# Performance work log

Hardware: AMD Instinct MI355X
Metric: run time of the kernel (lower is better)

## Reference

```python
import jax, jax.numpy as jnp
import numpy as np

B, T, E, H = 16, 4096, 384, 64

def setup_inputs() -> dict:
    key = jax.random.key(0)
    k1, k2, k3, k4 = jax.random.split(key, 4)
    x = jax.random.normal(k1, (B, T, E), dtype=jnp.float32)
    # nn.Linear default init ~ U(-1/sqrt(fan_in), 1/sqrt(fan_in)); scale normals similarly
    s = 1.0 / np.sqrt(E)
    Wk = jax.random.uniform(k2, (E, H), dtype=jnp.float32, minval=-s, maxval=s)
    Wq = jax.random.uniform(k3, (E, H), dtype=jnp.float32, minval=-s, maxval=s)
    Wv = jax.random.uniform(k4, (E, H), dtype=jnp.float32, minval=-s, maxval=s)
    return {"x": x, "Wk": Wk, "Wq": Wq, "Wv": Wv}

def reference(x, Wk, Wq, Wv):
    b, t, c = x.shape
    k = x @ Wk          # [b,t,h]
    q = x @ Wq          # [b,t,h]
    v = x @ Wv          # [b,t,h]
    # scale by C**-0.5 where C is the embedding dim (as in source)
    scale = c ** (-0.5)
    weights = jnp.einsum('bqh,bkh->bqk', q, k) * scale  # [b,t,t]
    causal = jnp.tril(jnp.ones((t, t), dtype=bool))
    weights = jnp.where(causal, weights, -jnp.inf)
    weights = jax.nn.softmax(weights, axis=-1)
    # dropout is identity in eval mode
    out = jnp.einsum('bqk,bkh->bqh', weights, v)          # [b,t,h]
    return out
```

## Files before the change

kernel.cpp:

```cpp
#include <hip/hip_runtime.h>
#include <hip/hip_bf16.h>
#include <math.h>


typedef __attribute__((ext_vector_type(4))) float f32x4;
typedef __attribute__((ext_vector_type(8))) __bf16 bf16x8;

#define DEVI static __device__ __forceinline__

DEVI unsigned short f2bf(float f) {
  union { float f; unsigned int u; } x; x.f = f;
  unsigned int r = x.u + 0x7fffu + ((x.u >> 16) & 1u);
  return (unsigned short)(r >> 16);
}

DEVI unsigned int cvtpk_bf16(float lo, float hi) {
  unsigned int r;
  asm("v_cvt_pk_bf16_f32 %0, %1, %2" : "=v"(r) : "v"(lo), "v"(hi));
  return r;
}

DEVI f32x4 mfma16(bf16x8 a, bf16x8 b, f32x4 c) {
  return __builtin_amdgcn_mfma_f32_16x16x32_bf16(a, b, c, 0, 0, 0);
}

DEVI bf16x8 lds_frag(const unsigned short* buf, int row, int gran) {
  return *(const bf16x8*)(buf + row * 64 + ((gran ^ (row & 7)) << 3));
}

DEVI void gl_lds16(const unsigned short* g, unsigned short* l) {
  __builtin_amdgcn_global_load_lds(
      (const __attribute__((address_space(1))) unsigned int*)g,
      (__attribute__((address_space(3))) unsigned int*)l, 16, 0, 0);
}

__global__ __launch_bounds__(256) void k_pack(const float* __restrict__ Wk,
                                              const float* __restrict__ Wq,
                                              const float* __restrict__ Wv,
                                              unsigned short* __restrict__ WT) {
  int idx = blockIdx.x * 256 + threadIdx.x;
  if (idx >= 192 * 384) return;
  int n = idx / 384, k = idx - n * 384;
  const float* W = (n < 64) ? Wk : ((n < 128) ? Wq : Wv);
  WT[idx] = f2bf(W[k * 64 + (n & 63)]);
}

__global__ __launch_bounds__(256, 4) void k_proj(const float* __restrict__ x,
                                                 const unsigned short* __restrict__ WT,
                                                 unsigned short* __restrict__ Y,
                                                 unsigned short* __restrict__ VT) {
  __shared__ __align__(16) unsigned short As[64 * 64];
  __shared__ __align__(16) unsigned short Bs[192 * 64];
  const int tid = threadIdx.x;
  const int lane = tid & 63, wid = tid >> 6;
  const int q = lane & 15, g = lane >> 4;
  const int wm = wid >> 1, wn = wid & 1;
  const int m0 = blockIdx.x * 64;

  f32x4 acc[2][6];
#pragma unroll
  for (int mt = 0; mt < 2; ++mt)
#pragma unroll
    for (int nt = 0; nt < 6; ++nt) acc[mt][nt] = f32x4{0.f, 0.f, 0.f, 0.f};

  const int ar = tid >> 2, ap = tid & 3;

  for (int ks = 0; ks < 6; ++ks) {
    const float4* xp = (const float4*)(x + (size_t)(m0 + ar) * 384 + ks * 64 + ap * 16);
#pragma unroll
    for (int cc = 0; cc < 2; ++cc) {
      float4 f0 = xp[cc * 2], f1 = xp[cc * 2 + 1];
      union { unsigned short h[8]; uint4 v; } u;
      u.h[0] = f2bf(f0.x); u.h[1] = f2bf(f0.y); u.h[2] = f2bf(f0.z); u.h[3] = f2bf(f0.w);
      u.h[4] = f2bf(f1.x); u.h[5] = f2bf(f1.y); u.h[6] = f2bf(f1.z); u.h[7] = f2bf(f1.w);
      int gran = ap * 2 + cc;
      *(uint4*)(As + ar * 64 + ((gran ^ (ar & 7)) << 3)) = u.v;
    }
#pragma unroll
    for (int i = 0; i < 6; ++i) {
      int c = tid + 256 * i;
      int row = c >> 3, gr = c & 7;
      uint4 w = *(const uint4*)(WT + (size_t)row * 384 + ks * 64 + gr * 8);
      *(uint4*)(Bs + row * 64 + ((gr ^ (row & 7)) << 3)) = w;
    }
    __syncthreads();
#pragma unroll
    for (int kk = 0; kk < 2; ++kk) {
      bf16x8 af[2], bfv[6];
#pragma unroll
      for (int mt = 0; mt < 2; ++mt) af[mt] = lds_frag(As, wm * 32 + mt * 16 + q, kk * 4 + g);
#pragma unroll
      for (int nt = 0; nt < 6; ++nt) bfv[nt] = lds_frag(Bs, wn * 96 + nt * 16 + q, kk * 4 + g);
#pragma unroll
      for (int mt = 0; mt < 2; ++mt)
#pragma unroll
        for (int nt = 0; nt < 6; ++nt) acc[mt][nt] = mfma16(af[mt], bfv[nt], acc[mt][nt]);
    }
    __syncthreads();
  }
#pragma unroll
  for (int mt = 0; mt < 2; ++mt) {
    const int mrow = m0 + wm * 32 + mt * 16 + g * 4;
#pragma unroll
    for (int nt = 0; nt < 6; ++nt) {
      const int ncol = wn * 96 + nt * 16 + q;
      if (wn == 1 && nt >= 2) {
        const int d = (nt - 2) * 16 + q;
        const int bb = mrow >> 12, t = mrow & 4095;
        uint2 pv;
        pv.x = cvtpk_bf16(acc[mt][nt][0], acc[mt][nt][1]);
        pv.y = cvtpk_bf16(acc[mt][nt][2], acc[mt][nt][3]);
        *(uint2*)(VT + (size_t)(bb * 64 + d) * 4096 + t) = pv;
      } else {
        size_t base = (size_t)mrow * 128 + ncol;
#pragma unroll
        for (int j = 0; j < 4; ++j) Y[base + (size_t)j * 128] = f2bf(acc[mt][nt][j]);
      }
    }
  }
}

__global__ __launch_bounds__(512, 4) void k_attn(const unsigned short* __restrict__ Y,
                                                 const unsigned short* __restrict__ VT,
                                                 float* __restrict__ out) {
  __shared__ __align__(16) unsigned short Ks[4][64 * 64];
  __shared__ __align__(16) unsigned short Vs[4][64 * 64];
  __shared__ __align__(16) unsigned short Ps[8][16 * 64];

  const int id = blockIdx.x;
  const int xcd = id & 7;
  const int b = xcd * 2 + ((id >> 3) & 1);
  const int rank = id >> 4;
  const int i = (rank < 16) ? (31 - rank) : (rank - 16);
  const int q0 = i * 128;
  const int nkv = 2 * i + 2;

  const int tid = threadIdx.x;
  const int lane = tid & 63, wid = tid >> 6;
  const int p = wid >> 2;
  const int w4 = wid & 3;
  const int q = lane & 15, g = lane >> 4;
  const float zsc = 0.073622223f;

  const unsigned short* Yb = Y + (size_t)b * 4096 * 128;
  const unsigned short* Vb = VT + (size_t)b * 64 * 4096;

#define STAGE(S, KV0)                                                           \
  {                                                                             \
    int r = tid >> 3, grs = (tid & 7) ^ (r & 7);                                \
    gl_lds16(Yb + (size_t)((KV0) + r) * 128 + grs * 8, Ks[S] + tid * 8);        \
    gl_lds16(Vb + (size_t)r * 4096 + (KV0) + grs * 8, Vs[S] + tid * 8);         \
  }

  STAGE(0, 0)
  STAGE(1, 64)
  __syncthreads();

  bf16x8 qf[2][2];
#pragma unroll
  for (int qh = 0; qh < 2; ++qh) {
    const unsigned short* qp = Yb + (size_t)(q0 + w4 * 32 + qh * 16 + q) * 128 + 64;
    bf16x8 r0 = *(const bf16x8*)(qp + g * 8);
    bf16x8 r1 = *(const bf16x8*)(qp + 32 + g * 8);
#pragma unroll
    for (int e = 0; e < 8; ++e) {
      r0[e] = (__bf16)((float)r0[e] * zsc);
      r1[e] = (__bf16)((float)r1[e] * zsc);
    }
    qf[qh][0] = r0; qf[qh][1] = r1;
  }

  f32x4 accO[2][4];
#pragma unroll
  for (int qh = 0; qh < 2; ++qh)
#pragma unroll
    for (int dt = 0; dt < 4; ++dt) accO[qh][dt] = f32x4{0.f, 0.f, 0.f, 0.f};
  float lsum[2] = {0.f, 0.f};

  const int mytiles = 2 * i + 1 + (w4 >> 1);
  const int nIt = nkv >> 1;

  for (int it = 0; it < nIt; ++it) {
    const int kt = 2 * it + p;
    const int t2 = 2 * it + 2, t3 = 2 * it + 3;
    if (t2 < nkv) STAGE(t2 & 3, t2 * 64)
    if (t3 < nkv) STAGE(t3 & 3, t3 * 64)

    if (kt < mytiles) {
      const int kv0 = kt * 64;
      const unsigned short* Kc = Ks[kt & 3];
      const unsigned short* Vc = Vs[kt & 3];

      bf16x8 ka0[4], ka1[4];
#pragma unroll
      for (int t = 0; t < 4; ++t) {
        ka0[t] = lds_frag(Kc, t * 16 + q, g);
        ka1[t] = lds_frag(Kc, t * 16 + q, 4 + g);
      }
      f32x4 accS[2][4];
      __builtin_amdgcn_s_setprio(1);
#pragma unroll
      for (int qh = 0; qh < 2; ++qh)
#pragma unroll
        for (int t = 0; t < 4; ++t) {
          f32x4 z = f32x4{0.f, 0.f, 0.f, 0.f};
          z = mfma16(ka0[t], qf[qh][0], z);
          z = mfma16(ka1[t], qf[qh][1], z);
          accS[qh][t] = z;
        }
      __builtin_amdgcn_s_setprio(0);

      const bool dmw = (kv0 + 63 >= q0 + w4 * 32);
      bf16x8 bp[2][2];
#pragma unroll
      for (int qh = 0; qh < 2; ++qh) {
        const int qrow = q0 + w4 * 32 + qh * 16 + q;
        if (dmw) {
#pragma unroll
          for (int t = 0; t < 4; ++t)
#pragma unroll
            for (int j = 0; j < 4; ++j)
              if (kv0 + t * 16 + g * 4 + j > qrow) accS[qh][t][j] = -INFINITY;
        }
        float ps0 = 0.f, ps1 = 0.f;
#pragma unroll
        for (int t = 0; t < 4; ++t) {
          float p0 = __builtin_amdgcn_exp2f(accS[qh][t][0]);
          float p1 = __builtin_amdgcn_exp2f(accS[qh][t][1]);
          float p2 = __builtin_amdgcn_exp2f(accS[qh][t][2]);
          float p3 = __builtin_amdgcn_exp2f(accS[qh][t][3]);
          ps0 += p0 + p1;
          ps1 += p2 + p3;
          uint2 pv;
          pv.x = cvtpk_bf16(p0, p1);
          pv.y = cvtpk_bf16(p2, p3);
          *(uint2*)(Ps[wid] + q * 64 + ((t * 16 + g * 4) ^ ((q & 7) << 3))) = pv;
        }
        lsum[qh] += ps0 + ps1;
        bp[qh][0] = lds_frag(Ps[wid], q, g);
        bp[qh][1] = lds_frag(Ps[wid], q, 4 + g);
      }

      __builtin_amdgcn_s_setprio(1);
#pragma unroll
      for (int dt = 0; dt < 4; ++dt) {
        bf16x8 av0 = lds_frag(Vc, dt * 16 + q, g);
        bf16x8 av1 = lds_frag(Vc, dt * 16 + q, 4 + g);
#pragma unroll
        for (int qh = 0; qh < 2; ++qh) {
          accO[qh][dt] = mfma16(av0, bp[qh][0], accO[qh][dt]);
          accO[qh][dt] = mfma16(av1, bp[qh][1], accO[qh][dt]);
        }
      }
      __builtin_amdgcn_s_setprio(0);
    }

    __syncthreads();
  }

#pragma unroll
  for (int qh = 0; qh < 2; ++qh) {
    lsum[qh] += __shfl_xor(lsum[qh], 16);
    lsum[qh] += __shfl_xor(lsum[qh], 32);
  }

  float* scrO = (float*)Ks;
  float* scrL = (float*)Vs;
  const int si = w4 * 64 + lane;
  if (p == 1) {
#pragma unroll
    for (int qh = 0; qh < 2; ++qh) {
      float* so = scrO + (si * 2 + qh) * 16;
#pragma unroll
      for (int dt = 0; dt < 4; ++dt) *(float4*)(so + dt * 4) = *(float4*)&accO[qh][dt];
      scrL[si * 2 + qh] = lsum[qh];
    }
  }
  __syncthreads();
  if (p == 0) {
#pragma unroll
    for (int qh = 0; qh < 2; ++qh) {
      const float* so = scrO + (si * 2 + qh) * 16;
      float rl = 1.0f / (lsum[qh] + scrL[si * 2 + qh]);
      const int qrow = q0 + w4 * 32 + qh * 16 + q;
      float* op = out + (size_t)(b * 4096 + qrow) * 64;
#pragma unroll
      for (int dt = 0; dt < 4; ++dt) {
        float4 ob = *(const float4*)(so + dt * 4);
        f32x4 vO;
        vO[0] = (accO[qh][dt][0] + ob.x) * rl;
        vO[1] = (accO[qh][dt][1] + ob.y) * rl;
        vO[2] = (accO[qh][dt][2] + ob.z) * rl;
        vO[3] = (accO[qh][dt][3] + ob.w) * rl;
        *(float4*)(op + dt * 16 + g * 4) = *(float4*)&vO;
      }
    }
  }
#undef STAGE
}

extern "C" void kernel_launch(void* const* d_in, const int* in_sizes, int n_in,
                              void* d_out, int out_size, void* d_ws, size_t ws_size,
                              hipStream_t stream) {
  const float* x  = (const float*)d_in[0];
  const float* Wk = (const float*)d_in[1];
  const float* Wq = (const float*)d_in[2];
  const float* Wv = (const float*)d_in[3];
  float* out = (float*)d_out;

  unsigned short* WT = (unsigned short*)d_ws;
  unsigned short* Y  = WT + 73728;
  unsigned short* VT = Y + 8388608;

  hipLaunchKernelGGL(k_pack, dim3(288), dim3(256), 0, stream, Wk, Wq, Wv, WT);
  hipLaunchKernelGGL(k_proj, dim3(1024), dim3(256), 0, stream, x, WT, Y, VT);
  hipLaunchKernelGGL(k_attn, dim3(512), dim3(512), 0, stream, Y, VT, out);
}
```

Measured before the change: 90.83 us.

## Halve attention query and KV tiles, compute row sums with an MFMA

The attention kernel now uses 64-row query blocks with 32-row KV tiles and 256-thread workgroups, launching twice as many blocks. LDS swizzles and staging addresses are reworked for the narrower tiles. The softmax denominator now comes from an extra MFMA against a ones-vector instead of scalar adds and cross-lane shuffles. The goals are finer causal load balance, less wasted masked work on diagonal tiles, and less VALU reduction work, at the cost of more blocks and more barrier overhead per KV element.

```diff
diff --git a/kernel.cpp b/kernel.cpp
--- a/kernel.cpp
+++ b/kernel.cpp
@@ -26,6 +26,10 @@
 
 DEVI bf16x8 lds_frag(const unsigned short* buf, int row, int gran) {
   return *(const bf16x8*)(buf + row * 64 + ((gran ^ (row & 7)) << 3));
+}
+
+DEVI bf16x8 lds_frag32(const unsigned short* buf, int row, int gran) {
+  return *(const bf16x8*)(buf + row * 32 + ((gran ^ ((row >> 1) & 3)) << 3));
 }
 
 DEVI void gl_lds16(const unsigned short* g, unsigned short* l) {
@@ -120,40 +124,42 @@
   }
 }
 
-__global__ __launch_bounds__(512, 4) void k_attn(const unsigned short* __restrict__ Y,
+__global__ __launch_bounds__(256, 4) void k_attn(const unsigned short* __restrict__ Y,
                                                  const unsigned short* __restrict__ VT,
                                                  float* __restrict__ out) {
-  __shared__ __align__(16) unsigned short Ks[4][64 * 64];
-  __shared__ __align__(16) unsigned short Vs[4][64 * 64];
-  __shared__ __align__(16) unsigned short Ps[8][16 * 64];
+  __shared__ __align__(16) unsigned short Ks[4][32 * 64];
+  __shared__ __align__(16) unsigned short Vs[4][64 * 32];
+  __shared__ __align__(16) unsigned short Ps[4][16 * 32];
 
   const int id = blockIdx.x;
-  const int xcd = id & 7;
-  const int b = xcd * 2 + ((id >> 3) & 1);
-  const int rank = id >> 4;
-  const int i = (rank < 16) ? (31 - rank) : (rank - 16);
-  const int q0 = i * 128;
+  const int xcd = id & 7, sub = id >> 3;
+  const int s = sub & 31, layer = sub >> 5;
+  const int b = xcd * 2 + (layer & 1);
+  const int i = (layer < 2) ? (63 - s) : s;
+  const int q0 = i * 64;
   const int nkv = 2 * i + 2;
 
   const int tid = threadIdx.x;
   const int lane = tid & 63, wid = tid >> 6;
-  const int p = wid >> 2;
-  const int w4 = wid & 3;
+  const int p = wid & 1;
+  const int w4 = wid >> 1;
   const int q = lane & 15, g = lane >> 4;
   const float zsc = 0.073622223f;
 
   const unsigned short* Yb = Y + (size_t)b * 4096 * 128;
   const unsigned short* Vb = VT + (size_t)b * 64 * 4096;
 
-#define STAGE(S, KV0)                                                           \
-  {                                                                             \
-    int r = tid >> 3, grs = (tid & 7) ^ (r & 7);                                \
-    gl_lds16(Yb + (size_t)((KV0) + r) * 128 + grs * 8, Ks[S] + tid * 8);        \
-    gl_lds16(Vb + (size_t)r * 4096 + (KV0) + grs * 8, Vs[S] + tid * 8);         \
+  const unsigned short* kSrc0 = Yb + (size_t)(tid >> 3) * 128 + (((tid & 7) ^ ((tid >> 3) & 7)) * 8);
+  const unsigned short* vSrc0 = Vb + (size_t)(tid >> 2) * 4096 + (((tid & 3) ^ ((tid >> 3) & 3)) * 8);
+
+#define STAGE(S, KT)                                          \
+  {                                                           \
+    gl_lds16(kSrc0 + (size_t)(KT) * 4096, Ks[S] + tid * 8);   \
+    gl_lds16(vSrc0 + (KT) * 32, Vs[S] + tid * 8);             \
   }
 
   STAGE(0, 0)
-  STAGE(1, 64)
+  STAGE(1, 1)
   __syncthreads();
 
   bf16x8 qf[2][2];
@@ -170,118 +176,123 @@
     qf[qh][0] = r0; qf[qh][1] = r1;
   }
 
-  f32x4 accO[2][4];
-#pragma unroll
-  for (int qh = 0; qh < 2; ++qh)
+  bf16x8 av1;
+  {
+    const unsigned short one = 0x3F80;
+    const unsigned short v = (q == 0) ? one : 0;
+#pragma unroll
+    for (int e = 0; e < 8; ++e) av1[e] = *(const __bf16*)&v;
+  }
+
+  f32x4 accO[2][4], accL[2];
+#pragma unroll
+  for (int qh = 0; qh < 2; ++qh) {
+    accL[qh] = f32x4{0.f, 0.f, 0.f, 0.f};
 #pragma unroll
     for (int dt = 0; dt < 4; ++dt) accO[qh][dt] = f32x4{0.f, 0.f, 0.f, 0.f};
-  float lsum[2] = {0.f, 0.f};
-
-  const int mytiles = 2 * i + 1 + (w4 >> 1);
-  const int nIt = nkv >> 1;
+  }
+
+  const int mytiles = 2 * i + w4 + 1;
+  const int dtile = 2 * i + w4;
+  const int nIt = i + 1;
+  unsigned short* Pw = Ps[wid];
 
   for (int it = 0; it < nIt; ++it) {
     const int kt = 2 * it + p;
     const int t2 = 2 * it + 2, t3 = 2 * it + 3;
-    if (t2 < nkv) STAGE(t2 & 3, t2 * 64)
-    if (t3 < nkv) STAGE(t3 & 3, t3 * 64)
+    if (t2 < nkv) STAGE(t2 & 3, t2)
+    if (t3 < nkv) STAGE(t3 & 3, t3)
 
     if (kt < mytiles) {
-      const int kv0 = kt * 64;
+      const int kv0 = kt * 32;
       const unsigned short* Kc = Ks[kt & 3];
       const unsigned short* Vc = Vs[kt & 3];
 
-      bf16x8 ka0[4], ka1[4];
-#pragma unroll
-      for (int t = 0; t < 4; ++t) {
-        ka0[t] = lds_frag(Kc, t * 16 + q, g);
-        ka1[t] = lds_frag(Kc, t * 16 + q, 4 + g);
-      }
-      f32x4 accS[2][4];
+      bf16x8 ka[2][2];
+#pragma unroll
+      for (int t = 0; t < 2; ++t) {
+        ka[t][0] = lds_frag(Kc, t * 16 + q, g);
+        ka[t][1] = lds_frag(Kc, t * 16 + q, 4 + g);
+      }
+      f32x4 accS[2][2];
       __builtin_amdgcn_s_setprio(1);
 #pragma unroll
       for (int qh = 0; qh < 2; ++qh)
 #pragma unroll
-        for (int t = 0; t < 4; ++t) {
+        for (int t = 0; t < 2; ++t) {
           f32x4 z = f32x4{0.f, 0.f, 0.f, 0.f};
-          z = mfma16(ka0[t], qf[qh][0], z);
-          z = mfma16(ka1[t], qf[qh][1], z);
+          z = mfma16(ka[t][0], qf[qh][0], z);
+          z = mfma16(ka[t][1], qf[qh][1], z);
           accS[qh][t] = z;
         }
       __builtin_amdgcn_s_setprio(0);
 
-      const bool dmw = (kv0 + 63 >= q0 + w4 * 32);
-      bf16x8 bp[2][2];
+      const bool dm = (kt == dtile);
+      bf16x8 bp[2];
 #pragma unroll
       for (int qh = 0; qh < 2; ++qh) {
-        const int qrow = q0 + w4 * 32 + qh * 16 + q;
-        if (dmw) {
-#pragma unroll
-          for (int t = 0; t < 4; ++t)
+        if (dm) {
+          const int qrow = q0 + w4 * 32 + qh * 16 + q;
+#pragma unroll
+          for (int t = 0; t < 2; ++t)
 #pragma unroll
             for (int j = 0; j < 4; ++j)
               if (kv0 + t * 16 + g * 4 + j > qrow) accS[qh][t][j] = -INFINITY;
         }
-        float ps0 = 0.f, ps1 = 0.f;
-#pragma unroll
-        for (int t = 0; t < 4; ++t) {
+#pragma unroll
+        for (int t = 0; t < 2; ++t) {
           float p0 = __builtin_amdgcn_exp2f(accS[qh][t][0]);
           float p1 = __builtin_amdgcn_exp2f(accS[qh][t][1]);
           float p2 = __builtin_amdgcn_exp2f(accS[qh][t][2]);
           float p3 = __builtin_amdgcn_exp2f(accS[qh][t][3]);
-          ps0 += p0 + p1;
-          ps1 += p2 + p3;
           uint2 pv;
           pv.x = cvtpk_bf16(p0, p1);
           pv.y = cvtpk_bf16(p2, p3);
-          *(uint2*)(Ps[wid] + q * 64 + ((t * 16 + g * 4) ^ ((q & 7) << 3))) = pv;
+          *(uint2*)(Pw + q * 32 + (((t * 2 + (g >> 1)) ^ ((q >> 1) & 3)) << 3) + (g & 1) * 4) = pv;
         }
-        lsum[qh] += ps0 + ps1;
-        bp[qh][0] = lds_frag(Ps[wid], q, g);
-        bp[qh][1] = lds_frag(Ps[wid], q, 4 + g);
+        asm volatile("" ::: "memory");
+        bp[qh] = lds_frag32(Pw, q, g);
+        asm volatile("" ::: "memory");
       }
 
       __builtin_amdgcn_s_setprio(1);
 #pragma unroll
       for (int dt = 0; dt < 4; ++dt) {
-        bf16x8 av0 = lds_frag(Vc, dt * 16 + q, g);
-        bf16x8 av1 = lds_frag(Vc, dt * 16 + q, 4 + g);
-#pragma unroll
-        for (int qh = 0; qh < 2; ++qh) {
-          accO[qh][dt] = mfma16(av0, bp[qh][0], accO[qh][dt]);
-          accO[qh][dt] = mfma16(av1, bp[qh][1], accO[qh][dt]);
-        }
-      }
+        bf16x8 av = lds_frag32(Vc, dt * 16 + q, g);
+#pragma unroll
+        for (int qh = 0; qh < 2; ++qh) accO[qh][dt] = mfma16(av, bp[qh], accO[qh][dt]);
+      }
+#pragma unroll
+      for (int qh = 0; qh < 2; ++qh) accL[qh] = mfma16(av1, bp[qh], accL[qh]);
       __builtin_amdgcn_s_setprio(0);
     }
 
     __syncthreads();
   }
-
-#pragma unroll
-  for (int qh = 0; qh < 2; ++qh) {
-    lsum[qh] += __shfl_xor(lsum[qh], 16);
-    lsum[qh] += __shfl_xor(lsum[qh], 32);
-  }
+#undef STAGE
+
+  float ls[2];
+#pragma unroll
+  for (int qh = 0; qh < 2; ++qh) ls[qh] = __shfl(accL[qh][0], lane & 15);
 
   float* scrO = (float*)Ks;
   float* scrL = (float*)Vs;
-  const int si = w4 * 64 + lane;
+  const int si = (w4 * 64 + lane) * 2;
   if (p == 1) {
 #pragma unroll
     for (int qh = 0; qh < 2; ++qh) {
-      float* so = scrO + (si * 2 + qh) * 16;
+      float* so = scrO + (si + qh) * 16;
 #pragma unroll
       for (int dt = 0; dt < 4; ++dt) *(float4*)(so + dt * 4) = *(float4*)&accO[qh][dt];
-      scrL[si * 2 + qh] = lsum[qh];
+      scrL[si + qh] = ls[qh];
     }
   }
   __syncthreads();
   if (p == 0) {
 #pragma unroll
     for (int qh = 0; qh < 2; ++qh) {
-      const float* so = scrO + (si * 2 + qh) * 16;
-      float rl = 1.0f / (lsum[qh] + scrL[si * 2 + qh]);
+      const float* so = scrO + (si + qh) * 16;
+      float rl = 1.0f / (ls[qh] + scrL[si + qh]);
       const int qrow = q0 + w4 * 32 + qh * 16 + q;
       float* op = out + (size_t)(b * 4096 + qrow) * 64;
 #pragma unroll
@@ -296,7 +307,6 @@
       }
     }
   }
-#undef STAGE
 }
 
 extern "C" void kernel_launch(void* const* d_in, const int* in_sizes, int n_in,
@@ -314,5 +324,5 @@
 
   hipLaunchKernelGGL(k_pack, dim3(288), dim3(256), 0, stream, Wk, Wq, Wv, WT);
   hipLaunchKernelGGL(k_proj, dim3(1024), dim3(256), 0, stream, x, WT, Y, VT);
-  hipLaunchKernelGGL(k_attn, dim3(512), dim3(512), 0, stream, Y, VT, out);
-}
+  hipLaunchKernelGGL(k_attn, dim3(1024), dim3(256), 0, stream, Y, VT, out);
+}
```

Measured after the change: 96.24 us. 6.0% more time.
